# Kernel tuning notes

Measured on AMD Instinct MI355X. Metric: run time of the kernel, lower is better.

Reference implementation:

```python
import jax, jax.numpy as jnp
import numpy as np

B, T, C = 16, 1024, 128  # batch, block_size (window length), n_hembd


def setup_inputs() -> dict:
    key = jax.random.key(0)
    k1, k2, k3 = jax.random.split(key, 3)
    Q = jax.random.normal(k1, (B, T, C), dtype=jnp.float32)
    K = jax.random.normal(k2, (B, 2 * T - 1, C), dtype=jnp.float32)
    # learned parameter keyWindowBias: (1, 1, n_hembd, block_size)
    bias = jax.random.normal(k3, (1, 1, C, T), dtype=jnp.float32)
    return {"Q": Q, "K": K, "bias": bias}


def reference(Q, K, bias):
    # Original: K_sw = K.unfold(1, T, 1) -> (B, T, C, T) with K_sw[b,w,c,t] = K[b,w+t,c]
    #           Z = einsum('bwc,bwct->bwt', Q, K_sw + bias)
    # Distribute the dot product over the bias add to avoid materializing (B,T,C,T):
    #   Z[b,w,t] = sum_c Q[b,w,c] * K[b,w+t,c]  +  sum_c Q[b,w,c] * bias[c,t]
    Bn, Tn, Cn = Q.shape
    # Dense scores against all 2T-1 key positions: (B, T, 2T-1)
    S = jnp.einsum('bwc,bkc->bwk', Q, K)
    # Gather sliding-window diagonals: idx[w, t] = w + t
    idx = jnp.arange(Tn)[:, None] + jnp.arange(Tn)[None, :]  # (T, T)
    Zk = jnp.take_along_axis(S, idx[None, :, :], axis=2)      # (B, T, T)
    # Bias contribution: Q @ bias, shared across windows
    Zb = jnp.einsum('bwc,ct->bwt', Q, bias[0, 0])             # (B, T, T)
    return Zk + Zb
```

## Files before the change

### kernel.cpp

```cpp
#include <hip/hip_runtime.h>
#include <hip/hip_bf16.h>


#define B_    16
#define T_    1024
#define C_    128
#define KT_   2047

#define BW    32
#define BT    64
#define KROWS 96
#define SS_LD 98
#define LDB   136

#define LDSS  130

typedef unsigned short ushort_t;
typedef short bf16x8 __attribute__((ext_vector_type(8)));
typedef float f32x4  __attribute__((ext_vector_type(4)));

__device__ __forceinline__ unsigned short f2bf(float f) {
  unsigned int u = __float_as_uint(f);
  u += 0x7FFFu + ((u >> 16) & 1u);
  return (unsigned short)(u >> 16);
}

__device__ __forceinline__ bf16x8 pack8(float4 lo, float4 hi) {
  bf16x8 r;
  r[0] = (short)f2bf(lo.x); r[1] = (short)f2bf(lo.y);
  r[2] = (short)f2bf(lo.z); r[3] = (short)f2bf(lo.w);
  r[4] = (short)f2bf(hi.x); r[5] = (short)f2bf(hi.y);
  r[6] = (short)f2bf(hi.z); r[7] = (short)f2bf(hi.w);
  return r;
}

typedef const __attribute__((address_space(1))) unsigned int* gas_ptr;
typedef __attribute__((address_space(3))) unsigned int* las_ptr;
__device__ __forceinline__ void async_copy16(const void* g, void* l) {
  __builtin_amdgcn_global_load_lds((gas_ptr)g, (las_ptr)l, 16, 0, 0);
}

__device__ __forceinline__ const bf16x8* frag(const ushort_t* t, int row, int kc) {
  return (const bf16x8*)(t + (((row << 4) + (kc ^ (row & 7))) << 3));
}

#define KN4 1048064
#define BN4 32768

__global__ __launch_bounds__(256) void prepass(
    const float* __restrict__ K, const float* __restrict__ bias,
    ushort_t* __restrict__ Kb, ushort_t* __restrict__ bT) {
  int idx = blockIdx.x * 256 + threadIdx.x;
  if (idx < KN4) {
    float4 v = ((const float4*)K)[idx];
    ((ushort4*)Kb)[idx] = make_ushort4(f2bf(v.x), f2bf(v.y), f2bf(v.z), f2bf(v.w));
  } else {
    int i = idx - KN4;
    int c = i >> 8;
    int g = i & 255;
    float4 v = ((const float4*)(bias + c * T_))[g];
    int t = g << 2;
    bT[(t + 0) * C_ + c] = f2bf(v.x);
    bT[(t + 1) * C_ + c] = f2bf(v.y);
    bT[(t + 2) * C_ + c] = f2bf(v.z);
    bT[(t + 3) * C_ + c] = f2bf(v.w);
  }
}

__global__ __launch_bounds__(512) void swmm_main(
    const float* __restrict__ Q, const ushort_t* __restrict__ Kb,
    const ushort_t* __restrict__ bT, float* __restrict__ out) {
  __shared__ __align__(16) ushort_t tile[5120 * 8];
  __shared__ __align__(16) float Ss[64 * LDSS];

  const int b    = blockIdx.x;
  const int w0   = blockIdx.y * 64;
  const int tid  = threadIdx.x;
  const int wv   = tid >> 6;
  const int lane = tid & 63;
  const int frow = lane & 15;
  const int quad = lane >> 4;
  const int mpair = wv & 1;
  const int wslot = wv >> 1;
  const int m0a = mpair * 16;
  const int m0b = m0a + 32;
  const int j0  = ((wslot + 1) & 3) * 16;

  const int r0 = tid >> 4;
  const int cc = (tid & 15) ^ (r0 & 7);
  const ushort_t* kbb = Kb + (size_t)b * KT_ * C_ + (cc << 3);
  const ushort_t* btb = bT + (cc << 3);

  auto stageK = [&](int chunk, int p) {
    int g0 = w0 + chunk * 64 + r0;
    int g1 = g0 + 32;
    if (g1 > KT_ - 1) g1 = KT_ - 1;
    async_copy16(kbb + (size_t)g0 * C_, &tile[(size_t)(p * 1024 + wv * 64) * 8]);
    async_copy16(kbb + (size_t)g1 * C_, &tile[(size_t)(p * 1024 + 512 + wv * 64) * 8]);
  };
  auto stageB = [&](int step, int q) {
    const ushort_t* g = btb + (size_t)(step * 64 + r0) * C_;
    async_copy16(g,           &tile[(size_t)(3072 + q * 1024 + wv * 64) * 8]);
    async_copy16(g + 32 * C_, &tile[(size_t)(3072 + q * 1024 + 512 + wv * 64) * 8]);
  };

  stageK(0, 0); stageK(1, 1); stageB(0, 0);

  bf16x8 aA[4], aB[4];
  {
    const float* qa = Q + ((size_t)(b * T_ + w0 + m0a + frow) << 7);
    const float* qb = qa + (32 << 7);
#pragma unroll
    for (int kk = 0; kk < 4; ++kk) {
      int co = (kk * 4 + quad) << 3;
      float4 lo = *(const float4*)(qa + co);
      float4 hi = *(const float4*)(qa + co + 4);
      aA[kk] = pack8(lo, hi);
      lo = *(const float4*)(qb + co);
      hi = *(const float4*)(qb + co + 4);
      aB[kk] = pack8(lo, hi);
    }
  }

  asm volatile("s_waitcnt vmcnt(0)" ::: "memory");
  __builtin_amdgcn_s_barrier();

  int p0 = 0, p1 = 1, p2 = 2;
  f32x4 baccA = {0.f, 0.f, 0.f, 0.f}, baccB = {0.f, 0.f, 0.f, 0.f};

  for (int s = 0; s < 16; ++s) {
    const int q0 = s & 1;

    if (s < 15) stageK(s + 2, p2);
    if (s < 15) stageB(s + 1, q0 ^ 1);

    __builtin_amdgcn_s_setprio(1);
#pragma unroll
    for (int ti = 0; ti < 3; ++ti) {
      const int t = wslot + ti * 4;
      if (t <= 6) {
        const int n0 = m0a + t * 16;
        const int pc = (n0 >> 6) ? p1 : p0;
        const int lrow = pc * 64 + ((n0 + frow) & 63);
        f32x4 accA = {0.f, 0.f, 0.f, 0.f};
        f32x4 accB = {0.f, 0.f, 0.f, 0.f};
#pragma unroll
        for (int kk = 0; kk < 4; ++kk) {
          bf16x8 bb = *frag(tile, lrow, kk * 4 + quad);
          if (t <= 4) accA = __builtin_amdgcn_mfma_f32_16x16x32_bf16(aA[kk], bb, accA, 0, 0, 0);
          if (t >= 2) accB = __builtin_amdgcn_mfma_f32_16x16x32_bf16(aB[kk], bb, accB, 0, 0, 0);
        }
        if (t <= 4) {
#pragma unroll
          for (int r = 0; r < 4; ++r)
            Ss[(m0a + quad * 4 + r) * LDSS + n0 + frow] = accA[r];
        }
        if (t >= 2) {
#pragma unroll
          for (int r = 0; r < 4; ++r)
            Ss[(m0b + quad * 4 + r) * LDSS + n0 + frow] = accB[r];
        }
      } else if (t <= 10) {
        const int brow = 192 + q0 * 64 + j0 + frow;
        f32x4 xA = {0.f, 0.f, 0.f, 0.f};
        f32x4 xB = {0.f, 0.f, 0.f, 0.f};
#pragma unroll
        for (int kk = 0; kk < 4; ++kk) {
          bf16x8 bb = *frag(tile, brow, kk * 4 + quad);
          xA = __builtin_amdgcn_mfma_f32_16x16x32_bf16(aA[kk], bb, xA, 0, 0, 0);
          xB = __builtin_amdgcn_mfma_f32_16x16x32_bf16(aB[kk], bb, xB, 0, 0, 0);
        }
        baccA = xA; baccB = xB;
      }
    }
    __builtin_amdgcn_s_setprio(0);

    asm volatile("s_waitcnt lgkmcnt(0)" ::: "memory");
    __builtin_amdgcn_s_barrier();
    asm volatile("s_waitcnt vmcnt(0)" ::: "memory");

    {
      float* op = out + ((size_t)(b * T_ + w0) * T_) + s * 64 + j0 + frow;
#pragma unroll
      for (int mi = 0; mi < 2; ++mi) {
        const int m = mi ? m0b : m0a;
        const f32x4 acc = mi ? baccB : baccA;
#pragma unroll
        for (int r = 0; r < 4; ++r) {
          const int i = m + quad * 4 + r;
          op[(size_t)i * T_] = acc[r] + Ss[i * LDSS + i + j0 + frow];
        }
      }
    }
    asm volatile("s_waitcnt lgkmcnt(0)" ::: "memory");
    __builtin_amdgcn_s_barrier();

    const int tp = p0; p0 = p1; p1 = p2; p2 = tp;
  }
}

__global__ __launch_bounds__(256) void swmm_fallback(
    const float* __restrict__ Q, const float* __restrict__ K,
    const float* __restrict__ bias, float* __restrict__ out) {
  __shared__ __align__(16) unsigned short Qs[BW * LDB];
  __shared__ __align__(16) unsigned short Ks[KROWS * LDB];
  __shared__ __align__(16) unsigned short Bs[BT * LDB];
  __shared__ __align__(16) float Ssf[BW * SS_LD];

  const int b   = blockIdx.z;
  const int w0  = blockIdx.y * BW;
  const int t0  = blockIdx.x * BT;
  const int kbase = w0 + t0;
  const int tid = threadIdx.x;

  {
    const float4* src = (const float4*)(Q + (size_t)(b * T_ + w0) * C_);
    for (int v = tid; v < BW * (C_ / 4); v += 256) {
      int r = v >> 5, cc = v & 31;
      float4 q = src[r * 32 + cc];
      unsigned short* d = &Qs[r * LDB + (cc << 2)];
      d[0] = f2bf(q.x); d[1] = f2bf(q.y); d[2] = f2bf(q.z); d[3] = f2bf(q.w);
    }
  }
  {
    for (int v = tid; v < KROWS * (C_ / 4); v += 256) {
      int r = v >> 5, cc = v & 31;
      int g = kbase + r;
      float4 kv = make_float4(0.f, 0.f, 0.f, 0.f);
      if (g < KT_) kv = ((const float4*)(K + ((size_t)b * KT_ + g) * C_))[cc];
      unsigned short* d = &Ks[r * LDB + (cc << 2)];
      d[0] = f2bf(kv.x); d[1] = f2bf(kv.y); d[2] = f2bf(kv.z); d[3] = f2bf(kv.w);
    }
  }
  {
    for (int v = tid; v < C_ * (BT / 4); v += 256) {
      int c = v >> 4, jj = v & 15;
      float4 bv = ((const float4*)(bias + (size_t)c * T_ + t0))[jj];
      int j4 = jj << 2;
      Bs[(j4 + 0) * LDB + c] = f2bf(bv.x);
      Bs[(j4 + 1) * LDB + c] = f2bf(bv.y);
      Bs[(j4 + 2) * LDB + c] = f2bf(bv.z);
      Bs[(j4 + 3) * LDB + c] = f2bf(bv.w);
    }
  }
  __syncthreads();

  const int wv    = tid >> 6;
  const int lane  = tid & 63;
  const int frow  = lane & 15;
  const int koff  = (lane >> 4) * 8;
  const int drow4 = (lane >> 4) * 4;
  const int NS = KROWS / 16;

  for (int s = wv; s < 2 * NS; s += 4) {
    int mb = s / NS, nn = s % NS;
    int m0 = mb * 16, n0 = nn * 16;
    const unsigned short* arow = &Qs[(m0 + frow) * LDB + koff];
    const unsigned short* brow = &Ks[(n0 + frow) * LDB + koff];
    f32x4 acc = {0.f, 0.f, 0.f, 0.f};
#pragma unroll
    for (int k0 = 0; k0 < C_; k0 += 32) {
      bf16x8 a  = *(const bf16x8*)(arow + k0);
      bf16x8 bb = *(const bf16x8*)(brow + k0);
      acc = __builtin_amdgcn_mfma_f32_16x16x32_bf16(a, bb, acc, 0, 0, 0);
    }
#pragma unroll
    for (int r = 0; r < 4; ++r)
      Ssf[(m0 + drow4 + r) * SS_LD + n0 + frow] = acc[r];
  }

  f32x4 bacc[2];
#pragma unroll
  for (int q = 0; q < 2; ++q) {
    int idx = wv + q * 4;
    int m0 = (idx >> 2) * 16, jj0 = (idx & 3) * 16;
    const unsigned short* arow = &Qs[(m0 + frow) * LDB + koff];
    const unsigned short* brow = &Bs[(jj0 + frow) * LDB + koff];
    f32x4 acc = {0.f, 0.f, 0.f, 0.f};
#pragma unroll
    for (int k0 = 0; k0 < C_; k0 += 32) {
      bf16x8 a  = *(const bf16x8*)(arow + k0);
      bf16x8 bb = *(const bf16x8*)(brow + k0);
      acc = __builtin_amdgcn_mfma_f32_16x16x32_bf16(a, bb, acc, 0, 0, 0);
    }
    bacc[q] = acc;
  }
  __syncthreads();

#pragma unroll
  for (int q = 0; q < 2; ++q) {
    int idx = wv + q * 4;
    int m0 = (idx >> 2) * 16, jj0 = (idx & 3) * 16;
#pragma unroll
    for (int r = 0; r < 4; ++r) {
      int i = m0 + drow4 + r;
      int j = jj0 + frow;
      out[(size_t)(b * T_ + w0 + i) * T_ + t0 + j] = bacc[q][r] + Ssf[i * SS_LD + i + j];
    }
  }
}

extern "C" void kernel_launch(void* const* d_in, const int* in_sizes, int n_in,
                              void* d_out, int out_size, void* d_ws, size_t ws_size,
                              hipStream_t stream) {
  const float* Q    = (const float*)d_in[0];
  const float* K    = (const float*)d_in[1];
  const float* bias = (const float*)d_in[2];
  float* out = (float*)d_out;

  const size_t KB = (size_t)B_ * KT_ * C_ * 2;
  const size_t TB = (size_t)T_ * C_ * 2;

  if (ws_size >= KB + TB) {
    ushort_t* Kb = (ushort_t*)d_ws;
    ushort_t* bT = (ushort_t*)((char*)d_ws + KB);
    prepass<<<(KN4 + BN4) / 256, 256, 0, stream>>>(K, bias, Kb, bT);
    swmm_main<<<dim3(B_, T_ / 64), dim3(512), 0, stream>>>(Q, Kb, bT, out);
  } else {
    swmm_fallback<<<dim3(T_ / BT, T_ / BW, B_), dim3(256), 0, stream>>>(Q, K, bias, out);
  }
}
```

Before: 116.1 us.

## Remap wave work so each wave computes one key column block for all rows

Reassigns the per-wave work split in the main kernel. Each of the 8 waves now holds Q fragments for all 64 window rows and computes one full 16-column band of the 128-wide key score tile, with every band-row pair run even where it is outside the useful diagonal. Each wave also computes the bias product for one column block and two row groups. This removes the irregular triangular scheduling and the branching across tile slots. The cost is more Q registers per wave (16 fragments instead of 8) and extra MFMA work on score entries the diagonal gather never reads.

```diff
diff --git a/kernel.cpp b/kernel.cpp
--- a/kernel.cpp
+++ b/kernel.cpp
@@ -80,11 +80,8 @@
   const int lane = tid & 63;
   const int frow = lane & 15;
   const int quad = lane >> 4;
-  const int mpair = wv & 1;
-  const int wslot = wv >> 1;
-  const int m0a = mpair * 16;
-  const int m0b = m0a + 32;
-  const int j0  = ((wslot + 1) & 3) * 16;
+  const int jb   = wv & 3;
+  const int mg   = wv >> 2;
 
   const int r0 = tid >> 4;
   const int cc = (tid & 15) ^ (r0 & 7);
@@ -106,19 +103,19 @@
 
   stageK(0, 0); stageK(1, 1); stageB(0, 0);
 
-  bf16x8 aA[4], aB[4];
+  bf16x8 a[4][4];
   {
-    const float* qa = Q + ((size_t)(b * T_ + w0 + m0a + frow) << 7);
-    const float* qb = qa + (32 << 7);
-#pragma unroll
-    for (int kk = 0; kk < 4; ++kk) {
-      int co = (kk * 4 + quad) << 3;
-      float4 lo = *(const float4*)(qa + co);
-      float4 hi = *(const float4*)(qa + co + 4);
-      aA[kk] = pack8(lo, hi);
-      lo = *(const float4*)(qb + co);
-      hi = *(const float4*)(qb + co + 4);
-      aB[kk] = pack8(lo, hi);
+    const float* qp = Q + ((size_t)(b * T_ + w0 + frow) << 7);
+#pragma unroll
+    for (int mi = 0; mi < 4; ++mi) {
+      const float* qm = qp + ((size_t)(mi * 16) << 7);
+#pragma unroll
+      for (int kk = 0; kk < 4; ++kk) {
+        int co = (kk * 4 + quad) << 3;
+        float4 lo = *(const float4*)(qm + co);
+        float4 hi = *(const float4*)(qm + co + 4);
+        a[mi][kk] = pack8(lo, hi);
+      }
     }
   }
 
@@ -135,44 +132,41 @@
     if (s < 15) stageB(s + 1, q0 ^ 1);
 
     __builtin_amdgcn_s_setprio(1);
-#pragma unroll
-    for (int ti = 0; ti < 3; ++ti) {
-      const int t = wslot + ti * 4;
-      if (t <= 6) {
-        const int n0 = m0a + t * 16;
-        const int pc = (n0 >> 6) ? p1 : p0;
-        const int lrow = pc * 64 + ((n0 + frow) & 63);
-        f32x4 accA = {0.f, 0.f, 0.f, 0.f};
-        f32x4 accB = {0.f, 0.f, 0.f, 0.f};
-#pragma unroll
-        for (int kk = 0; kk < 4; ++kk) {
-          bf16x8 bb = *frag(tile, lrow, kk * 4 + quad);
-          if (t <= 4) accA = __builtin_amdgcn_mfma_f32_16x16x32_bf16(aA[kk], bb, accA, 0, 0, 0);
-          if (t >= 2) accB = __builtin_amdgcn_mfma_f32_16x16x32_bf16(aB[kk], bb, accB, 0, 0, 0);
-        }
-        if (t <= 4) {
-#pragma unroll
-          for (int r = 0; r < 4; ++r)
-            Ss[(m0a + quad * 4 + r) * LDSS + n0 + frow] = accA[r];
-        }
-        if (t >= 2) {
-#pragma unroll
-          for (int r = 0; r < 4; ++r)
-            Ss[(m0b + quad * 4 + r) * LDSS + n0 + frow] = accB[r];
-        }
-      } else if (t <= 10) {
-        const int brow = 192 + q0 * 64 + j0 + frow;
-        f32x4 xA = {0.f, 0.f, 0.f, 0.f};
-        f32x4 xB = {0.f, 0.f, 0.f, 0.f};
-#pragma unroll
-        for (int kk = 0; kk < 4; ++kk) {
-          bf16x8 bb = *frag(tile, brow, kk * 4 + quad);
-          xA = __builtin_amdgcn_mfma_f32_16x16x32_bf16(aA[kk], bb, xA, 0, 0, 0);
-          xB = __builtin_amdgcn_mfma_f32_16x16x32_bf16(aB[kk], bb, xB, 0, 0, 0);
-        }
-        baccA = xA; baccB = xB;
+
+    {
+      const int n0 = wv * 16;
+      const int pc = (wv >= 4) ? p1 : p0;
+      const int lrow = pc * 64 + ((n0 + frow) & 63);
+      f32x4 acc[4];
+#pragma unroll
+      for (int mi = 0; mi < 4; ++mi) acc[mi] = (f32x4){0.f, 0.f, 0.f, 0.f};
+#pragma unroll
+      for (int kk = 0; kk < 4; ++kk) {
+        bf16x8 bb = *frag(tile, lrow, kk * 4 + quad);
+#pragma unroll
+        for (int mi = 0; mi < 4; ++mi)
+          acc[mi] = __builtin_amdgcn_mfma_f32_16x16x32_bf16(a[mi][kk], bb, acc[mi], 0, 0, 0);
       }
-    }
+#pragma unroll
+      for (int mi = 0; mi < 4; ++mi)
+#pragma unroll
+        for (int r = 0; r < 4; ++r)
+          Ss[(mi * 16 + quad * 4 + r) * LDSS + n0 + frow] = acc[mi][r];
+    }
+
+    {
+      const int brow = 192 + q0 * 64 + jb * 16 + frow;
+      f32x4 xA = {0.f, 0.f, 0.f, 0.f};
+      f32x4 xB = {0.f, 0.f, 0.f, 0.f};
+#pragma unroll
+      for (int kk = 0; kk < 4; ++kk) {
+        bf16x8 bb = *frag(tile, brow, kk * 4 + quad);
+        xA = __builtin_amdgcn_mfma_f32_16x16x32_bf16(a[2 * mg + 0][kk], bb, xA, 0, 0, 0);
+        xB = __builtin_amdgcn_mfma_f32_16x16x32_bf16(a[2 * mg + 1][kk], bb, xB, 0, 0, 0);
+      }
+      baccA = xA; baccB = xB;
+    }
+
     __builtin_amdgcn_s_setprio(0);
 
     asm volatile("s_waitcnt lgkmcnt(0)" ::: "memory");
@@ -180,15 +174,15 @@
     asm volatile("s_waitcnt vmcnt(0)" ::: "memory");
 
     {
-      float* op = out + ((size_t)(b * T_ + w0) * T_) + s * 64 + j0 + frow;
-#pragma unroll
-      for (int mi = 0; mi < 2; ++mi) {
-        const int m = mi ? m0b : m0a;
-        const f32x4 acc = mi ? baccB : baccA;
+      float* op = out + ((size_t)(b * T_ + w0) * T_) + s * 64 + jb * 16 + frow;
+#pragma unroll
+      for (int pi = 0; pi < 2; ++pi) {
+        const int mi = 2 * mg + pi;
+        const f32x4 acc = pi ? baccB : baccA;
 #pragma unroll
         for (int r = 0; r < 4; ++r) {
-          const int i = m + quad * 4 + r;
-          op[(size_t)i * T_] = acc[r] + Ss[i * LDSS + i + j0 + frow];
+          const int i = mi * 16 + quad * 4 + r;
+          op[(size_t)i * T_] = acc[r] + Ss[i * LDSS + i + jb * 16 + frow];
         }
       }
     }
```

Measured after the change: 129.4 us. 1.11x slower.
